# Performance work log

Hardware: AMD Instinct MI355X
Metric: run time of the kernel (lower is better)

Reference implementation:

```python
import jax, jax.numpy as jnp
import numpy as np

B, W, F = 32, 100, 128   # batch, window_size, n_features
KSIZE = 7                # conv kernel size
EMB = 8                  # embedding dim for feature-similarity matrix
ALPHA = 0.2              # leaky relu negative slope


def setup_inputs() -> dict:
    key = jax.random.key(0)
    ks = jax.random.split(key, 10)
    s = 0.05
    return {
        "x": jax.random.normal(ks[0], (B, W, F), jnp.float32),
        # ConvLayer: Conv1d(F, F, KSIZE) with 'same' padding
        "conv_w": jax.random.normal(ks[1], (F, F, KSIZE), jnp.float32) * s,
        "conv_b": jnp.zeros((F,), jnp.float32),
        # TemporalAttentionLayer (GATv2): lin(2F -> 2F), a (2F,1), bias (W,W)
        "temp_lin_w": jax.random.normal(ks[2], (2 * F, 2 * F), jnp.float32) * s,
        "temp_lin_b": jnp.zeros((2 * F,), jnp.float32),
        "temp_a": jax.random.normal(ks[3], (2 * F, 1), jnp.float32) * s,
        "temp_bias": jnp.zeros((W, W), jnp.float32),
        # FeatureAttentionLayer (GATv2): lin(2W -> 2W), a (2W,1), bias (F,F)
        "feat_lin_w": jax.random.normal(ks[4], (2 * W, 2 * W), jnp.float32) * s,
        "feat_lin_b": jnp.zeros((2 * W,), jnp.float32),
        "feat_a": jax.random.normal(ks[5], (2 * W, 1), jnp.float32) * s,
        "feat_bias": jnp.zeros((F, F), jnp.float32),
        # nn.Embedding(F, EMB) table (indexed by arange(F) -> just the table)
        "emb": jax.random.normal(ks[6], (F, EMB), jnp.float32),
        # forecasting model: Linear(W, 1) + tanh
        "fc_w": jax.random.normal(ks[7], (1, W), jnp.float32) * s,
        "fc_b": jnp.zeros((1,), jnp.float32),
    }


def _pos_encode(x):
    # pe = sin(pos*div) + cos(pos*div), div = exp(arange(F) * -ln(1e4)/F)
    pos = jnp.arange(W, dtype=jnp.float32)[:, None]
    div = jnp.exp(jnp.arange(F, dtype=jnp.float32) * (-np.log(10000.0) / F))
    pe = jnp.sin(pos * div) + jnp.cos(pos * div)  # (W, F)
    return x + pe[None]


def _conv(x, w, b):
    # x: (B, W, F) -> Conv1d over time with channels = features, 'same' length
    xc = x.transpose(0, 2, 1)  # (B, F, W)
    pad = (KSIZE - 1) // 2
    y = jax.lax.conv_general_dilated(
        xc, w, window_strides=(1,), padding=[(pad, pad)],
        dimension_numbers=("NCW", "OIW", "NCW"))
    y = jax.nn.relu(y + b[None, :, None])
    return y.transpose(0, 2, 1)  # (B, W, F)


def _gat_v2(v, lin_w, lin_b, a, bias):
    # v: (B, K, D). Equivalent to lin(concat(v_i, v_j)) via split weights +
    # broadcast add (avoids the O(K^2) concat materialization).
    D = v.shape[-1]
    left = v @ lin_w[:, :D].T    # (B, K, E) -- v_i part
    right = v @ lin_w[:, D:].T   # (B, K, E) -- v_j part
    s = left[:, :, None, :] + right[:, None, :, :] + lin_b  # (B, K, K, E)
    s = jnp.where(s >= 0, s, ALPHA * s)  # leaky relu
    e = jnp.einsum("bije,e->bij", s, a[:, 0]) + bias  # (B, K, K)
    att = jax.nn.softmax(e, axis=2)
    return jnp.tanh(jnp.einsum("bij,bjd->bid", att, v))


def reference(x, conv_w, conv_b, temp_lin_w, temp_lin_b, temp_a, temp_bias,
              feat_lin_w, feat_lin_b, feat_a, feat_bias, emb, fc_w, fc_b):
    x = _pos_encode(x)                 # (B, W, F)
    x = _conv(x, conv_w, conv_b)       # (B, W, F)
    # temporal attention: nodes = time steps
    x = _gat_v2(x, temp_lin_w, temp_lin_b, temp_a, temp_bias)  # (B, W, F)
    # feature attention: nodes = features
    xf = x.transpose(0, 2, 1)          # (B, F, W)
    xf = _gat_v2(xf, feat_lin_w, feat_lin_b, feat_a, feat_bias)
    x = xf.transpose(0, 2, 1)          # (B, W, F)
    # cosine-similarity mixing over features
    norms = jnp.linalg.norm(emb, axis=-1)
    cos = (emb @ emb.T) / (norms[:, None] * norms[None, :])  # (F, F)
    x = x @ cos.T                      # (B, W, F)
    xp = x.transpose(0, 2, 1)          # (B, F, W)
    pred = jnp.tanh(xp @ fc_w.T + fc_b)  # (B, F, 1)
    return pred.transpose(0, 2, 1)     # (B, 1, F)
```

## Files before the change

kernel.cpp:

```cpp
#include <hip/hip_runtime.h>
#include <math.h>

#define BB 32
#define WW 100
#define FF 128
#define KS 7
#define ET 256
#define EF 200


__global__ void k_prep(const float* __restrict__ cw, const float* __restrict__ tlw,
                       const float* __restrict__ flw, float* __restrict__ wt,
                       float* __restrict__ tlwT, float* __restrict__ flwT,
                       int* __restrict__ cnt) {
    int id = blockIdx.x * 256 + threadIdx.x;
    if (id < 32) cnt[id] = 0;
    if (id < KS * FF * FF) {
        int o = id & (FF - 1);
        int r = id >> 7;
        int k = r % KS;
        int i = r / KS;
        wt[id] = cw[(o * FF + i) * KS + k];
    }
    if (id < ET * ET) {
        int e = id & (ET - 1);
        int d = id >> 8;
        tlwT[id] = tlw[e * ET + d];
    }
    if (id < EF * EF) {
        int e = id % EF;
        int d = id / EF;
        flwT[id] = flw[e * EF + d];
    }
}

#define CTW 10
#define NROW 16
#define XPAD 20
__global__ __launch_bounds__(512) void k_conv(const float* __restrict__ x,
                                              const float* __restrict__ wt,
                                              const float* __restrict__ cb,
                                              const float* __restrict__ tlwT,
                                              const float* __restrict__ tlb,
                                              float* __restrict__ x2,
                                              float* __restrict__ LT,
                                              float* __restrict__ Rt) {
    int b = blockIdx.x & 31;
    int tile = blockIdx.x >> 5;
    int w0 = tile * CTW;
    int tid = threadIdx.x;
    int o = tid & (FF - 1);
    int h = tid >> 7;
    __shared__ float xs[FF][XPAD];
    __shared__ float part[4][CTW][FF];
    __shared__ float xs2[CTW][FF];
    for (int idx = tid; idx < NROW * FF; idx += 512) {
        int r = idx >> 7, f = idx & (FF - 1);
        int t = w0 - 3 + r;
        float v = 0.f;
        if ((unsigned)t < WW) {
            float div = __expf((float)f * (-9.210340371976184f / (float)FF));
            float arg = (float)t * div;
            v = x[(b * WW + t) * FF + f] + __sinf(arg) + __cosf(arg);
        }
        xs[f][r] = v;
    }
    __syncthreads();
    float acc[CTW];
#pragma unroll
    for (int t = 0; t < CTW; ++t) acc[t] = 0.f;
    const float* wbase = wt + (h * 32) * KS * FF + o;
#pragma unroll 2
    for (int il = 0; il < 32; ++il) {
        int i = h * 32 + il;
        float4 X0 = *(const float4*)&xs[i][0];
        float4 X1 = *(const float4*)&xs[i][4];
        float4 X2 = *(const float4*)&xs[i][8];
        float4 X3 = *(const float4*)&xs[i][12];
        float xr[16] = {X0.x, X0.y, X0.z, X0.w, X1.x, X1.y, X1.z, X1.w,
                        X2.x, X2.y, X2.z, X2.w, X3.x, X3.y, X3.z, X3.w};
        const float* wp = wbase + il * KS * FF;
#pragma unroll
        for (int k = 0; k < KS; ++k) {
            float wv = wp[k * FF];
#pragma unroll
            for (int t = 0; t < CTW; ++t) acc[t] += xr[t + k] * wv;
        }
    }
#pragma unroll
    for (int t = 0; t < CTW; ++t) part[h][t][o] = acc[t];
    __syncthreads();
    for (int idx = tid; idx < CTW * FF; idx += 512) {
        int t = idx >> 7, oo = idx & (FF - 1);
        float s = part[0][t][oo] + part[1][t][oo] + part[2][t][oo] +
                  part[3][t][oo] + cb[oo];
        s = fmaxf(s, 0.f);
        x2[(b * WW + w0 + t) * FF + oo] = s;
        xs2[t][oo] = s;
    }
    __syncthreads();
    int e = tid & 255;
    int rh = tid >> 8;
    float aL[5] = {0, 0, 0, 0, 0}, aR[5] = {0, 0, 0, 0, 0};
    const float* wl = tlwT + e;
#pragma unroll 2
    for (int dc = 0; dc < 32; ++dc) {
        float xv[5][4];
#pragma unroll
        for (int r = 0; r < 5; ++r)
            *(float4*)xv[r] = *(const float4*)&xs2[rh * 5 + r][dc * 4];
#pragma unroll
        for (int q = 0; q < 4; ++q) {
            int d = dc * 4 + q;
            float wL = wl[d * ET];
            float wR = wl[(FF + d) * ET];
#pragma unroll
            for (int r = 0; r < 5; ++r) {
                aL[r] += xv[r][q] * wL;
                aR[r] += xv[r][q] * wR;
            }
        }
    }
    float lb = tlb[e];
    int ibase = w0 + rh * 5;
    float* Lp = LT + (b * ET + e) * WW + ibase;
    float* Rp = Rt + (b * ET + e) * WW + ibase;
#pragma unroll
    for (int r = 0; r < 5; ++r) {
        Lp[r] = aL[r] + lb;
        Rp[r] = aR[r];
    }
}

__global__ __launch_bounds__(512) void k_att_t(const float* __restrict__ LT,
                                               const float* __restrict__ Rt,
                                               const float* __restrict__ ta,
                                               const float* __restrict__ tbias,
                                               const float* __restrict__ x2,
                                               float* __restrict__ x3T) {
    int b = blockIdx.x & 31;
    int tile = blockIdx.x >> 5;
    int i0 = tile * 8;
    int tid = threadIdx.x;
    int j = tid & 127, g = tid >> 7;
    __shared__ float Rs[2][32][FF];
    __shared__ float Ls[2][32][8];
    __shared__ float tas[ET];
    __shared__ float attQ[8][FF];
    __shared__ float ob[8][FF];
    __shared__ float redA[8][2], redB[8][2];
    if (tid < ET) tas[tid] = ta[tid];

    float rv[8];
    float lvr = 0.f;
    {
        const float* Rb = Rt + (b * ET) * WW;
#pragma unroll
        for (int it = 0; it < 8; ++it) {
            int idx = tid + it * 512;
            int er = idx >> 7, w = idx & 127;
            rv[it] = (w < WW) ? Rb[er * WW + w] : 0.f;
        }
        if (tid < 256) {
            int er = tid >> 3, qq = tid & 7;
            int row = i0 + qq; if (row >= WW) row = WW - 1;
            lvr = LT[(b * ET + er) * WW + row];
        }
    }
#pragma unroll
    for (int it = 0; it < 8; ++it) {
        int idx = tid + it * 512;
        Rs[0][idx >> 7][idx & 127] = rv[it];
    }
    if (tid < 256) Ls[0][tid >> 3][tid & 7] = lvr;
    __syncthreads();

    float s0 = 0.f, s1 = 0.f;
    for (int ch = 0; ch < 8; ++ch) {
        int buf = ch & 1;
        if (ch < 7) {
            int e0 = (ch + 1) * 32;
            const float* Rb = Rt + (b * ET + e0) * WW;
#pragma unroll
            for (int it = 0; it < 8; ++it) {
                int idx = tid + it * 512;
                int er = idx >> 7, w = idx & 127;
                rv[it] = (w < WW) ? Rb[er * WW + w] : 0.f;
            }
            if (tid < 256) {
                int er = tid >> 3, qq = tid & 7;
                int row = i0 + qq; if (row >= WW) row = WW - 1;
                lvr = LT[(b * ET + e0 + er) * WW + row];
            }
        }
        int e0 = ch * 32;
#pragma unroll 8
        for (int e = 0; e < 32; ++e) {
            float rj = Rs[buf][e][j];
            float ae = tas[e0 + e];
            float2 lv2 = *(const float2*)&Ls[buf][e][g * 2];
            float v;
            v = lv2.x + rj; v = fmaxf(v, 0.2f * v); s0 += v * ae;
            v = lv2.y + rj; v = fmaxf(v, 0.2f * v); s1 += v * ae;
        }
        if (ch < 7) {
#pragma unroll
            for (int it = 0; it < 8; ++it) {
                int idx = tid + it * 512;
                Rs[buf ^ 1][idx >> 7][idx & 127] = rv[it];
            }
            if (tid < 256) Ls[buf ^ 1][tid >> 3][tid & 7] = lvr;
        }
        __syncthreads();
    }

    float ej[2];
    {
        int iq = i0 + g * 2;
        float bv0 = (j < WW && iq < WW) ? tbias[iq * WW + j] : 0.f;
        float bv1 = (j < WW && iq + 1 < WW) ? tbias[(iq + 1) * WW + j] : 0.f;
        ej[0] = (j < WW && iq < WW) ? s0 + bv0 : -1e30f;
        ej[1] = (j < WW && iq + 1 < WW) ? s1 + bv1 : -1e30f;
    }
    float m[2] = {ej[0], ej[1]};
#pragma unroll
    for (int off = 32; off > 0; off >>= 1) {
#pragma unroll
        for (int ii = 0; ii < 2; ++ii) m[ii] = fmaxf(m[ii], __shfl_xor(m[ii], off));
    }
    int wv = tid >> 6;
    if ((tid & 63) == 0) { redA[wv][0] = m[0]; redA[wv][1] = m[1]; }
    __syncthreads();
    float p[2], ps[2];
#pragma unroll
    for (int ii = 0; ii < 2; ++ii) {
        float mx = fmaxf(redA[g * 2][ii], redA[g * 2 + 1][ii]);
        p[ii] = (j < WW) ? __expf(ej[ii] - mx) : 0.f;
        ps[ii] = p[ii];
    }
#pragma unroll
    for (int off = 32; off > 0; off >>= 1) {
#pragma unroll
        for (int ii = 0; ii < 2; ++ii) ps[ii] += __shfl_xor(ps[ii], off);
    }
    if ((tid & 63) == 0) { redB[wv][0] = ps[0]; redB[wv][1] = ps[1]; }
    __syncthreads();
#pragma unroll
    for (int ii = 0; ii < 2; ++ii) {
        float inv = 1.f / (redB[g * 2][ii] + redB[g * 2 + 1][ii]);
        attQ[g * 2 + ii][j] = p[ii] * inv;
    }

    int d = j, ph = g;
    float pv0 = 0.f, pv1 = 0.f;
#pragma unroll
    for (int it = 0; it < 8; ++it) {
        int idx = tid + it * 512;
        int r = idx >> 7, f = idx & 127;
        rv[it] = (r < WW) ? x2[(b * WW + r) * FF + f] : 0.f;
    }
    __syncthreads();
#pragma unroll
    for (int it = 0; it < 8; ++it) {
        int idx = tid + it * 512;
        Rs[0][idx >> 7][idx & 127] = rv[it];
    }
    __syncthreads();
    const float* a0 = attQ[ph * 2];
    const float* a1 = attQ[ph * 2 + 1];
    for (int jc = 0; jc < 4; ++jc) {
        int buf = jc & 1;
        if (jc < 3) {
            int r0 = (jc + 1) * 32;
#pragma unroll
            for (int it = 0; it < 8; ++it) {
                int idx = tid + it * 512;
                int r = idx >> 7, f = idx & 127;
                int row = r0 + r;
                rv[it] = (row < WW) ? x2[(b * WW + row) * FF + f] : 0.f;
            }
        }
#pragma unroll 8
        for (int r = 0; r < 32; ++r) {
            float xv = Rs[buf][r][d];
            int row = jc * 32 + r;
            pv0 += a0[row] * xv;
            pv1 += a1[row] * xv;
        }
        if (jc < 3) {
#pragma unroll
            for (int it = 0; it < 8; ++it) {
                int idx = tid + it * 512;
                Rs[buf ^ 1][idx >> 7][idx & 127] = rv[it];
            }
        }
        __syncthreads();
    }
    ob[ph * 2][d] = tanhf(pv0);
    ob[ph * 2 + 1][d] = tanhf(pv1);
    __syncthreads();
    if (tid < 256) {
        int f = tid >> 1, half = tid & 1;
        if (i0 + half * 4 < WW) {
            float4 v = make_float4(ob[half * 4][f], ob[half * 4 + 1][f],
                                   ob[half * 4 + 2][f], ob[half * 4 + 3][f]);
            *(float4*)&x3T[(b * FF + f) * WW + i0 + half * 4] = v;
        }
    }
}

__global__ __launch_bounds__(512) void k_lr_f(const float* __restrict__ x3T,
                                              const float* __restrict__ flwT,
                                              const float* __restrict__ flb,
                                              float* __restrict__ LfT,
                                              float* __restrict__ RfT) {
    int b = blockIdx.x & 31;
    int tile = blockIdx.x >> 5;
    int f0 = tile * 8;
    int tid = threadIdx.x;
    int e = tid & 255;
    int rh = tid >> 8;
    __shared__ float xs[8][WW];
    for (int idx = tid; idx < 8 * WW; idx += 512) {
        int r = idx / WW, d = idx % WW;
        xs[r][d] = x3T[(b * FF + f0 + r) * WW + d];
    }
    __syncthreads();
    if (e < EF) {
        float aL[4] = {0, 0, 0, 0}, aR[4] = {0, 0, 0, 0};
        const float* wl = flwT + e;
#pragma unroll 2
        for (int dc = 0; dc < 25; ++dc) {
            float xv[4][4];
#pragma unroll
            for (int r = 0; r < 4; ++r)
                *(float4*)xv[r] = *(const float4*)&xs[rh * 4 + r][dc * 4];
#pragma unroll
            for (int q = 0; q < 4; ++q) {
                int d = dc * 4 + q;
                float wL = wl[d * EF];
                float wR = wl[(WW + d) * EF];
#pragma unroll
                for (int r = 0; r < 4; ++r) {
                    aL[r] += xv[r][q] * wL;
                    aR[r] += xv[r][q] * wR;
                }
            }
        }
        float lb = flb[e];
        float o0[4];
#pragma unroll
        for (int r = 0; r < 4; ++r) o0[r] = aL[r] + lb;
        int fbase = f0 + rh * 4;
        *(float4*)&LfT[(b * EF + e) * FF + fbase] = *(float4*)o0;
        *(float4*)&RfT[(b * EF + e) * FF + fbase] = *(float4*)aR;
    }
}

__global__ __launch_bounds__(512) void k_att_f(const float* __restrict__ LfT,
                                               const float* __restrict__ RfT,
                                               const float* __restrict__ fa,
                                               const float* __restrict__ fbias,
                                               const float* __restrict__ x3T,
                                               const float* __restrict__ fcw,
                                               const float* __restrict__ emb,
                                               const float* __restrict__ fcb,
                                               float* __restrict__ tj,
                                               int* __restrict__ cnt,
                                               float* __restrict__ out) {
    int b = blockIdx.x & 31;
    int tile = blockIdx.x >> 5;
    int f0 = tile * 8;
    int tid = threadIdx.x;
    int j = tid & 127, g = tid >> 7;
    __shared__ float Rs[2][40][FF];
    __shared__ float Ls[2][40][8];
    __shared__ float fas[EF];
    __shared__ float attQ[8][FF];
    __shared__ float redA[8][2], redB[8][2], redT[8][2];
    __shared__ float en[FF][12];
    __shared__ float tjs2[FF];
    __shared__ int isLast;
    if (tid < EF) fas[tid] = fa[tid];

    float rv[10];
    float lvr = 0.f;
    {
        const float* Rb = RfT + (b * EF) * FF;
#pragma unroll
        for (int it = 0; it < 10; ++it) {
            int idx = tid + it * 512;
            rv[it] = Rb[idx];
        }
        if (tid < 320) {
            int er = tid >> 3, qq = tid & 7;
            lvr = LfT[(b * EF + er) * FF + f0 + qq];
        }
    }
#pragma unroll
    for (int it = 0; it < 10; ++it) {
        int idx = tid + it * 512;
        Rs[0][idx >> 7][idx & 127] = rv[it];
    }
    if (tid < 320) Ls[0][tid >> 3][tid & 7] = lvr;
    __syncthreads();

    float s0 = 0.f, s1 = 0.f;
    for (int ch = 0; ch < 5; ++ch) {
        int buf = ch & 1;
        if (ch < 4) {
            int e0 = (ch + 1) * 40;
            const float* Rb = RfT + (b * EF + e0) * FF;
#pragma unroll
            for (int it = 0; it < 10; ++it) {
                int idx = tid + it * 512;
                rv[it] = Rb[idx];
            }
            if (tid < 320) {
                int er = tid >> 3, qq = tid & 7;
                lvr = LfT[(b * EF + e0 + er) * FF + f0 + qq];
            }
        }
        int e0 = ch * 40;
#pragma unroll 8
        for (int e = 0; e < 40; ++e) {
            float rj = Rs[buf][e][j];
            float ae = fas[e0 + e];
            float2 lv2 = *(const float2*)&Ls[buf][e][g * 2];
            float v;
            v = lv2.x + rj; v = fmaxf(v, 0.2f * v); s0 += v * ae;
            v = lv2.y + rj; v = fmaxf(v, 0.2f * v); s1 += v * ae;
        }
        if (ch < 4) {
#pragma unroll
            for (int it = 0; it < 10; ++it) {
                int idx = tid + it * 512;
                Rs[buf ^ 1][idx >> 7][idx & 127] = rv[it];
            }
            if (tid < 320) Ls[buf ^ 1][tid >> 3][tid & 7] = lvr;
        }
        __syncthreads();
    }

    float ej[2] = {s0 + fbias[(f0 + g * 2) * FF + j],
                   s1 + fbias[(f0 + g * 2 + 1) * FF + j]};
    float m[2] = {ej[0], ej[1]};
#pragma unroll
    for (int off = 32; off > 0; off >>= 1) {
#pragma unroll
        for (int ii = 0; ii < 2; ++ii) m[ii] = fmaxf(m[ii], __shfl_xor(m[ii], off));
    }
    int wv = tid >> 6;
    if ((tid & 63) == 0) { redA[wv][0] = m[0]; redA[wv][1] = m[1]; }
    __syncthreads();
    float p[2], ps[2];
#pragma unroll
    for (int ii = 0; ii < 2; ++ii) {
        float mx = fmaxf(redA[g * 2][ii], redA[g * 2 + 1][ii]);
        p[ii] = __expf(ej[ii] - mx);
        ps[ii] = p[ii];
    }
#pragma unroll
    for (int off = 32; off > 0; off >>= 1) {
#pragma unroll
        for (int ii = 0; ii < 2; ++ii) ps[ii] += __shfl_xor(ps[ii], off);
    }
    if ((tid & 63) == 0) { redB[wv][0] = ps[0]; redB[wv][1] = ps[1]; }
    __syncthreads();
#pragma unroll
    for (int ii = 0; ii < 2; ++ii) {
        float inv = 1.f / (redB[g * 2][ii] + redB[g * 2 + 1][ii]);
        attQ[g * 2 + ii][j] = p[ii] * inv;
    }

    int w = j, ph = g;
    float pv0 = 0.f, pv1 = 0.f;
#pragma unroll
    for (int it = 0; it < 8; ++it) {
        int idx = tid + it * 512;
        int r = idx >> 7, ww = idx & 127;
        rv[it] = (ww < WW) ? x3T[(b * FF + r) * WW + ww] : 0.f;
    }
    __syncthreads();
#pragma unroll
    for (int it = 0; it < 8; ++it) {
        int idx = tid + it * 512;
        Rs[0][idx >> 7][idx & 127] = rv[it];
    }
    __syncthreads();
    const float* a0 = attQ[ph * 2];
    const float* a1 = attQ[ph * 2 + 1];
    for (int jc = 0; jc < 4; ++jc) {
        int buf = jc & 1;
        if (jc < 3) {
            int r0 = (jc + 1) * 32;
#pragma unroll
            for (int it = 0; it < 8; ++it) {
                int idx = tid + it * 512;
                int r = idx >> 7, ww = idx & 127;
                rv[it] = (ww < WW) ? x3T[(b * FF + r0 + r) * WW + ww] : 0.f;
            }
        }
#pragma unroll 8
        for (int r = 0; r < 32; ++r) {
            float xv = Rs[buf][r][w];
            int row = jc * 32 + r;
            pv0 += a0[row] * xv;
            pv1 += a1[row] * xv;
        }
        if (jc < 3) {
#pragma unroll
            for (int it = 0; it < 8; ++it) {
                int idx = tid + it * 512;
                Rs[buf ^ 1][idx >> 7][idx & 127] = rv[it];
            }
        }
        __syncthreads();
    }
    bool wok = (w < WW);
    float fcv = wok ? fcw[w] : 0.f;
    float tv[2] = {tanhf(pv0) * fcv, tanhf(pv1) * fcv};
#pragma unroll
    for (int off = 32; off > 0; off >>= 1) {
#pragma unroll
        for (int ii = 0; ii < 2; ++ii) tv[ii] += __shfl_xor(tv[ii], off);
    }
    if ((tid & 63) == 0) { redT[wv][0] = tv[0]; redT[wv][1] = tv[1]; }
    __syncthreads();
    if (tid < 8) {
        int q = tid, php = q >> 1, ii = q & 1;
        tj[b * FF + f0 + q] = redT[php * 2][ii] + redT[php * 2 + 1][ii];
    }
    __syncthreads();
    if (tid == 0) {
        __threadfence();
        int old = atomicAdd(&cnt[b], 1);
        isLast = (old == 15);
    }
    __syncthreads();
    if (isLast) {
        __threadfence();
        if (tid < 128) {
            int f = tid;
            float4 e0 = *(const float4*)&emb[f * 8];
            float4 e1 = *(const float4*)&emb[f * 8 + 4];
            float n = e0.x*e0.x + e0.y*e0.y + e0.z*e0.z + e0.w*e0.w +
                      e1.x*e1.x + e1.y*e1.y + e1.z*e1.z + e1.w*e1.w;
            float rin = rsqrtf(n);
            en[f][0] = e0.x*rin; en[f][1] = e0.y*rin;
            en[f][2] = e0.z*rin; en[f][3] = e0.w*rin;
            en[f][4] = e1.x*rin; en[f][5] = e1.y*rin;
            en[f][6] = e1.z*rin; en[f][7] = e1.w*rin;
            tjs2[f] = tj[b * FF + f];
        }
        __syncthreads();
        if (tid < 128) {
            int f = tid;
            float er[8];
#pragma unroll
            for (int k = 0; k < 8; ++k) er[k] = en[f][k];
            float acc = fcb[0];
            for (int jj = 0; jj < FF; ++jj) {
                float4 a = *(const float4*)&en[jj][0];
                float4 c = *(const float4*)&en[jj][4];
                float d8 = er[0]*a.x + er[1]*a.y + er[2]*a.z + er[3]*a.w +
                           er[4]*c.x + er[5]*c.y + er[6]*c.z + er[7]*c.w;
                acc += d8 * tjs2[jj];
            }
            out[b * FF + f] = tanhf(acc);
        }
    }
}

extern "C" void kernel_launch(void* const* d_in, const int* in_sizes, int n_in,
                              void* d_out, int out_size, void* d_ws, size_t ws_size,
                              hipStream_t stream) {
    const float* x     = (const float*)d_in[0];
    const float* cw    = (const float*)d_in[1];
    const float* cb    = (const float*)d_in[2];
    const float* tlw   = (const float*)d_in[3];
    const float* tlb   = (const float*)d_in[4];
    const float* ta    = (const float*)d_in[5];
    const float* tbias = (const float*)d_in[6];
    const float* flw   = (const float*)d_in[7];
    const float* flb   = (const float*)d_in[8];
    const float* fa    = (const float*)d_in[9];
    const float* fbias = (const float*)d_in[10];
    const float* emb   = (const float*)d_in[11];
    const float* fcw   = (const float*)d_in[12];
    const float* fcb   = (const float*)d_in[13];
    float* out = (float*)d_out;
    float* ws = (float*)d_ws;

    float* x2   = ws + 409600;
    float* x3T  = ws + 819200;
    float* LT   = ws + 1228800;
    float* Rt   = ws + 2048000;
    float* tj   = ws + 2867200;
    int*   cnt  = (int*)(ws + 2871296);
    float* wt   = ws + 3297280;
    float* tlwT = ws + 3411968;
    float* flwT = ws + 3477504;

    k_prep<<<448, 256, 0, stream>>>(cw, tlw, flw, wt, tlwT, flwT, cnt);
    k_conv<<<BB * 10, 512, 0, stream>>>(x, wt, cb, tlwT, tlb, x2, LT, Rt);
    k_att_t<<<BB * 13, 512, 0, stream>>>(LT, Rt, ta, tbias, x2, x3T);
    k_lr_f<<<BB * 16, 512, 0, stream>>>(x3T, flwT, flb, LT, Rt);
    k_att_f<<<BB * 16, 512, 0, stream>>>(LT, Rt, fa, fbias, x3T, fcw,
                                         emb, fcb, tj, cnt, out);
}
```

Baseline: 123.6 us.

## Split temporal linear projection out of conv kernel into separate k_lr_t kernel

Moves the temporal GATv2 linear projection (L/R) out of the conv kernel into its own kernel, which reads x2 back from global memory and works on 8-row tiles with float4 stores. The conv kernel becomes smaller, with less shared memory and fewer registers, which may raise occupancy. In exchange it adds a kernel launch and a global round trip of x2. Each thread now handles 4 rows instead of 5, and the last tile clamps reads past row 100 and skips those writes.

New measurement: 126.4 us. +2.2%, slower.

```diff
diff --git a/kernel.cpp b/kernel.cpp
--- a/kernel.cpp
+++ b/kernel.cpp
@@ -40,11 +40,7 @@
 __global__ __launch_bounds__(512) void k_conv(const float* __restrict__ x,
                                               const float* __restrict__ wt,
                                               const float* __restrict__ cb,
-                                              const float* __restrict__ tlwT,
-                                              const float* __restrict__ tlb,
-                                              float* __restrict__ x2,
-                                              float* __restrict__ LT,
-                                              float* __restrict__ Rt) {
+                                              float* __restrict__ x2) {
     int b = blockIdx.x & 31;
     int tile = blockIdx.x >> 5;
     int w0 = tile * CTW;
@@ -53,7 +49,6 @@
     int h = tid >> 7;
     __shared__ float xs[FF][XPAD];
     __shared__ float part[4][CTW][FF];
-    __shared__ float xs2[CTW][FF];
     for (int idx = tid; idx < NROW * FF; idx += 512) {
         int r = idx >> 7, f = idx & (FF - 1);
         int t = w0 - 3 + r;
@@ -94,41 +89,56 @@
         int t = idx >> 7, oo = idx & (FF - 1);
         float s = part[0][t][oo] + part[1][t][oo] + part[2][t][oo] +
                   part[3][t][oo] + cb[oo];
-        s = fmaxf(s, 0.f);
-        x2[(b * WW + w0 + t) * FF + oo] = s;
-        xs2[t][oo] = s;
-    }
-    __syncthreads();
+        x2[(b * WW + w0 + t) * FF + oo] = fmaxf(s, 0.f);
+    }
+}
+
+__global__ __launch_bounds__(512) void k_lr_t(const float* __restrict__ x2,
+                                              const float* __restrict__ tlwT,
+                                              const float* __restrict__ tlb,
+                                              float* __restrict__ LT,
+                                              float* __restrict__ Rt) {
+    int b = blockIdx.x & 31;
+    int tile = blockIdx.x >> 5;
+    int i0 = tile * 8;
+    int tid = threadIdx.x;
     int e = tid & 255;
     int rh = tid >> 8;
-    float aL[5] = {0, 0, 0, 0, 0}, aR[5] = {0, 0, 0, 0, 0};
+    __shared__ float xs[8][FF];
+    for (int idx = tid; idx < 8 * FF; idx += 512) {
+        int r = idx >> 7, d = idx & (FF - 1);
+        int row = i0 + r; if (row >= WW) row = WW - 1;
+        xs[r][d] = x2[(b * WW + row) * FF + d];
+    }
+    __syncthreads();
+    float aL[4] = {0, 0, 0, 0}, aR[4] = {0, 0, 0, 0};
     const float* wl = tlwT + e;
 #pragma unroll 2
     for (int dc = 0; dc < 32; ++dc) {
-        float xv[5][4];
-#pragma unroll
-        for (int r = 0; r < 5; ++r)
-            *(float4*)xv[r] = *(const float4*)&xs2[rh * 5 + r][dc * 4];
+        float xv[4][4];
+#pragma unroll
+        for (int r = 0; r < 4; ++r)
+            *(float4*)xv[r] = *(const float4*)&xs[rh * 4 + r][dc * 4];
 #pragma unroll
         for (int q = 0; q < 4; ++q) {
             int d = dc * 4 + q;
             float wL = wl[d * ET];
             float wR = wl[(FF + d) * ET];
 #pragma unroll
-            for (int r = 0; r < 5; ++r) {
+            for (int r = 0; r < 4; ++r) {
                 aL[r] += xv[r][q] * wL;
                 aR[r] += xv[r][q] * wR;
             }
         }
     }
-    float lb = tlb[e];
-    int ibase = w0 + rh * 5;
-    float* Lp = LT + (b * ET + e) * WW + ibase;
-    float* Rp = Rt + (b * ET + e) * WW + ibase;
-#pragma unroll
-    for (int r = 0; r < 5; ++r) {
-        Lp[r] = aL[r] + lb;
-        Rp[r] = aR[r];
+    int ibase = i0 + rh * 4;
+    if (ibase < WW) {
+        float lb = tlb[e];
+        float o0[4];
+#pragma unroll
+        for (int r = 0; r < 4; ++r) o0[r] = aL[r] + lb;
+        *(float4*)&LT[(b * ET + e) * WW + ibase] = *(float4*)o0;
+        *(float4*)&Rt[(b * ET + e) * WW + ibase] = *(float4*)aR;
     }
 }
 
@@ -603,7 +613,8 @@
     float* flwT = ws + 3477504;
 
     k_prep<<<448, 256, 0, stream>>>(cw, tlw, flw, wt, tlwT, flwT, cnt);
-    k_conv<<<BB * 10, 512, 0, stream>>>(x, wt, cb, tlwT, tlb, x2, LT, Rt);
+    k_conv<<<BB * 10, 512, 0, stream>>>(x, wt, cb, x2);
+    k_lr_t<<<BB * 13, 512, 0, stream>>>(x2, tlwT, tlb, LT, Rt);
     k_att_t<<<BB * 13, 512, 0, stream>>>(LT, Rt, ta, tbias, x2, x3T);
     k_lr_f<<<BB * 16, 512, 0, stream>>>(x3T, flwT, flb, LT, Rt);
     k_att_f<<<BB * 16, 512, 0, stream>>>(LT, Rt, fa, fbias, x3T, fcw,
```
